# Kernel tuning notes

Hardware: AMD Instinct MI355X
Metric: run time of the kernel (lower is better)

Reference implementation:

```python
import jax, jax.numpy as jnp
import numpy as np
from jax import lax

DIVISOR = 2.0

def setup_inputs() -> dict:
    key = jax.random.key(0)
    k1, k2, k3, k4 = jax.random.split(key, 4)
    x = jax.random.normal(k1, (32, 3, 32, 128, 128), dtype=jnp.float16)
    conv_w = jax.random.normal(k2, (16, 3, 3, 3, 3), dtype=jnp.float16) * 0.1
    conv_b = jax.random.normal(k3, (16,), dtype=jnp.float16)
    bias = jax.random.normal(k4, (16,), dtype=jnp.float16)
    return {"x": x, "conv_w": conv_w, "conv_b": conv_b, "bias": bias}

def reference(x, conv_w, conv_b, bias):
    # Conv3d (valid padding, stride 1), fp16 like conv.half()
    y = lax.conv_general_dilated(
        x, conv_w, window_strides=(1, 1, 1), padding="VALID",
        dimension_numbers=("NCDHW", "OIDHW", "NCDHW"))
    y = y + conv_b[None, :, None, None, None]
    # Fused ReLU + 2x2x2 max pool
    y = jnp.maximum(y, jnp.asarray(0, y.dtype))
    B, C, D, H, W = y.shape
    Dp, Hp, Wp = D // 2, H // 2, W // 2
    pooled = y[:, :, :2 * Dp, :2 * Hp, :2 * Wp].reshape(
        B, C, Dp, 2, Hp, 2, Wp, 2).max(axis=(3, 5, 7))  # [B,C,Dp,Hp,Wp]
    # Spatial mean in fp32 (kernel accumulates in float)
    avg = pooled.astype(jnp.float32).mean(axis=(2, 3, 4))  # [B,C]
    # /divisor + bias[c], then sum over channels -> [B,1,1,1]
    per_ch = avg / DIVISOR + bias.astype(jnp.float32)[None, :]
    return per_ch.sum(axis=1).reshape(B, 1, 1, 1)
```

## Files before the change

kernel.cpp:

```cpp
#include <hip/hip_runtime.h>
#include <hip/hip_bf16.h>


typedef __attribute__((ext_vector_type(8)))  short  short8;
typedef __attribute__((ext_vector_type(2)))  float  floatx2;
typedef __attribute__((ext_vector_type(4)))  float  floatx4;
typedef __attribute__((ext_vector_type(16))) float  floatx16;

__device__ __forceinline__ short f2bf(float f) {
    unsigned u = __builtin_bit_cast(unsigned, f);
    unsigned r = (u + 0x7FFFu + ((u >> 16) & 1u)) >> 16;
    return (short)r;
}

__device__ __forceinline__ unsigned pkbf2(float a, float b) {
    __hip_bfloat162 h = __float22bfloat162_rn(float2{a, b});
    unsigned r;
    __builtin_memcpy(&r, &h, 4);
    return r;
}

template <int CTRL>
__device__ __forceinline__ float dpp_max(float v) {
    int x = __builtin_bit_cast(int, v);
    int y = __builtin_amdgcn_mov_dpp(x, CTRL, 0xF, 0xF, true);
    return fmaxf(v, __builtin_bit_cast(float, y));
}

#define BAR() asm volatile("s_waitcnt lgkmcnt(0)\n\ts_barrier" ::: "memory")

#define BUFSZ 16640

__global__ void init_kernel(const float* __restrict__ wg,
                            const float* __restrict__ biasg,
                            short* __restrict__ wtab,
                            float* __restrict__ out)
{
    const int t = threadIdx.x;
    if (t < 576) {
        const int lane = t & 63, f = t >> 6;
        const int kh = f / 3, kw = f % 3;
        const int m = lane & 31, hs = lane >> 5;
        const int ch = m >> 1, dd = m & 1;
        short8 v;
        #pragma unroll
        for (int j = 0; j < 8; ++j) {
            const int s = hs * 8 + j;
            const int dl = s >> 2, ci = s & 3;
            const int kd = dl - dd;
            v[j] = (ci < 3 && kd >= 0 && kd < 3)
                 ? f2bf(wg[ch * 81 + ci * 27 + kd * 9 + kh * 3 + kw]) : (short)0;
        }
        ((short8*)wtab)[f * 64 + lane] = v;
    }
    if (t < 32) {
        float s = 0.f;
        #pragma unroll
        for (int cc = 0; cc < 16; ++cc) s += biasg[cc];
        out[t] = s;
    }
}

__global__ __launch_bounds__(512, 4) void fused_conv_pool_reduce(
    const float* __restrict__ xg,
    const short* __restrict__ wtab,
    const float* __restrict__ cbg,
    float* __restrict__ out)
{
    __shared__ __align__(16) short rawT[2 * 130 * 64];
    __shared__ float wsums[8];

    const int lin = blockIdx.y * 63 + blockIdx.x;
    const int nl  = (lin & 7) * 252 + (lin >> 3);
    const int hp  = nl % 63;
    const int b   = nl / 63;

    const int tid = threadIdx.x;
    const int lane = tid & 63;
    const int wv   = tid >> 6;
    const int hs   = lane >> 5;

    short8 af[9];
    #pragma unroll
    for (int f = 0; f < 9; ++f) af[f] = ((const short8*)wtab)[f * 64 + lane];
    const float cbv = cbg[(lane >> 1) & 15];
    float maskA[4];
    #pragma unroll
    for (int a = 0; a < 4; ++a) {
        const bool ok = ((lane & 1) == 0) && (wv * 8 + 2 * a + hs <= 62);
        maskA[a] = ok ? 1.0f : 0.0f;
    }

    if (tid < 64)
        *(unsigned long long*)((char*)rawT + (tid >> 5) * BUFSZ + 16384 + (tid & 31) * 8) = 0ULL;

    #define SWZ(r) (((r) ^ ((r) >> 3)) & 7)

    const int w4 = tid & 31, dr2 = (tid >> 5) & 1, rr = (tid >> 6) & 1, hr2 = (tid >> 7) & 3;
    int waddr2[2];
    #pragma unroll
    for (int j = 0; j < 2; ++j) {
        const int row = 2 * w4 + 64 * rr + j;
        waddr2[j] = row * 128 + ((hr2 * 2) ^ SWZ(row)) * 16 + dr2 * 8;
    }

    const int wi = (lane >> 1) & 15, hh = lane & 1;
    int raddr[3][3];
    #pragma unroll
    for (int kh = 0; kh < 3; ++kh) {
        #pragma unroll
        for (int kw = 0; kw < 3; ++kw) {
            const int row = wv * 16 + wi + kw;
            const int phys = ((hh + kh) * 2 + hs) ^ SWZ(row);
            raddr[kh][kw] = row * 128 + phys * 16;
        }
    }

    {
        const int w4p = tid & 31, drp = (tid >> 5) & 3, hrp = (tid >> 7) & 3;
        const float* srcP = xg + ((size_t)b * 96 + drp) * 16384 + (2 * hp + hrp) * 128 + 4 * w4p;
        const floatx4 c0 = *(const floatx4*)(srcP);
        const floatx4 c1 = *(const floatx4*)(srcP + 524288);
        const floatx4 c2 = *(const floatx4*)(srcP + 1048576);
        const int chunkL = hrp * 2 + (drp >> 1);
        #pragma unroll
        for (int i = 0; i < 4; ++i) {
            const int row = 4 * w4p + i;
            const int ad = row * 128 + (chunkL ^ SWZ(row)) * 16 + (drp & 1) * 8;
            uint2 pk;
            pk.x = pkbf2(c0[i], c1[i]);
            pk.y = pkbf2(c2[i], 0.0f);
            *(uint2*)((char*)rawT + ad) = pk;
        }
    }

    const float* src2 = xg + ((size_t)b * 96 + 4 + dr2) * 16384
                      + (2 * hp + hr2) * 128 + 2 * w4 + 64 * rr;
    floatx2 A0 = *(const floatx2*)(src2);
    floatx2 A1 = *(const floatx2*)(src2 + 524288);
    floatx2 A2 = *(const floatx2*)(src2 + 1048576);

    float vsum = 0.f;
    for (int dp = 0; dp < 15; ++dp) {
        const int p16 = (dp & 1) << 4;
        if (dp <= 13) {
            const int bw = (((dp >> 1) + 1) & 1) * BUFSZ;
            uint2 pk0, pk1;
            pk0.x = pkbf2(A0[0], A1[0]); pk0.y = pkbf2(A2[0], 0.0f);
            pk1.x = pkbf2(A0[1], A1[1]); pk1.y = pkbf2(A2[1], 0.0f);
            *(uint2*)((char*)rawT + bw + (waddr2[0] ^ p16)) = pk0;
            *(uint2*)((char*)rawT + bw + (waddr2[1] ^ p16)) = pk1;
            if (dp <= 12) {
                src2 += 32768;
                A0 = *(const floatx2*)(src2);
                A1 = *(const floatx2*)(src2 + 524288);
                A2 = *(const floatx2*)(src2 + 1048576);
            }
        }
        BAR();

        const int roff = (((dp + hs) >> 1) & 1) * BUFSZ;

        floatx16 acc = {0.f,0.f,0.f,0.f,0.f,0.f,0.f,0.f,
                        0.f,0.f,0.f,0.f,0.f,0.f,0.f,0.f};
        #pragma unroll
        for (int kh = 0; kh < 3; ++kh) {
            #pragma unroll
            for (int kw = 0; kw < 3; ++kw) {
                const short8 bf = *(const short8*)((char*)rawT + roff + (raddr[kh][kw] ^ p16));
                acc = __builtin_amdgcn_mfma_f32_32x32x16_bf16(bf, af[kh * 3 + kw], acc, 0, 0, 0);
            }
        }
        #pragma unroll
        for (int a = 0; a < 4; ++a) {
            float m01 = fmaxf(acc[4 * a],     acc[4 * a + 1]);
            float m23 = fmaxf(acc[4 * a + 2], acc[4 * a + 3]);
            float m   = fmaxf(m01, m23);
            m = dpp_max<0xB1>(m);
            const float v = fmaxf(m + cbv, 0.f);
            vsum = fmaf(maskA[a], v, vsum);
        }
    }

    float s = vsum;
    #pragma unroll
    for (int off = 1; off < 64; off <<= 1) s += __shfl_xor(s, off, 64);

    if (lane == 0) wsums[wv] = s;
    __syncthreads();
    if (tid == 0) {
        float bs = 0.f;
        #pragma unroll
        for (int i = 0; i < 8; ++i) bs += wsums[i];
        atomicAdd(&out[b], bs * (1.0f / 119070.0f));
    }
}

extern "C" void kernel_launch(void* const* d_in, const int* in_sizes, int n_in,
                              void* d_out, int out_size, void* d_ws, size_t ws_size,
                              hipStream_t stream) {
    const float* x      = (const float*)d_in[0];
    const float* conv_w = (const float*)d_in[1];
    const float* conv_b = (const float*)d_in[2];
    const float* bias   = (const float*)d_in[3];
    float* out = (float*)d_out;
    short* wtab = (short*)d_ws;

    init_kernel<<<1, 576, 0, stream>>>(conv_w, bias, wtab, out);
    dim3 grid(63, 32);
    fused_conv_pool_reduce<<<grid, 512, 0, stream>>>(x, wtab, conv_b, out);
}
```

Baseline: 287.2 us.

## Reuse kh=0/2 LDS fragments to synthesize kh=1 via DPP, unroll loop by two

The kernel now reads two LDS fragments per kw (kh=0 and kh=2) and builds the kh=1 fragment by swapping adjacent lanes with DPP, where it used to do three separate LDS reads. This cuts LDS read traffic per MFMA step by a third. The depth loop is also unrolled in pairs with precomputed even/odd read and write addresses, which removes the per-iteration XOR and branch logic. The cost is extra VALU selects and DPP moves per fragment, plus more address registers, and correctness depends on the lane pairing matching the LDS layout.

```diff
diff --git a/kernel.cpp b/kernel.cpp
--- a/kernel.cpp
+++ b/kernel.cpp
@@ -5,6 +5,7 @@
 typedef __attribute__((ext_vector_type(8)))  short  short8;
 typedef __attribute__((ext_vector_type(2)))  float  floatx2;
 typedef __attribute__((ext_vector_type(4)))  float  floatx4;
+typedef __attribute__((ext_vector_type(4)))  int    intx4;
 typedef __attribute__((ext_vector_type(16))) float  floatx16;
 
 __device__ __forceinline__ short f2bf(float f) {
@@ -25,6 +26,18 @@
     int x = __builtin_bit_cast(int, v);
     int y = __builtin_amdgcn_mov_dpp(x, CTRL, 0xF, 0xF, true);
     return fmaxf(v, __builtin_bit_cast(float, y));
+}
+
+__device__ __forceinline__ short8 mixF1(short8 f0, short8 f2, bool hh1) {
+    intx4 a = __builtin_bit_cast(intx4, f0);
+    intx4 b = __builtin_bit_cast(intx4, f2);
+    intx4 r;
+    #pragma unroll
+    for (int i = 0; i < 4; ++i) {
+        int s = hh1 ? a[i] : b[i];
+        r[i] = __builtin_amdgcn_mov_dpp(s, 0xB1, 0xF, 0xF, true);
+    }
+    return __builtin_bit_cast(short8, r);
 }
 
 #define BAR() asm volatile("s_waitcnt lgkmcnt(0)\n\ts_barrier" ::: "memory")
@@ -90,6 +103,7 @@
         const bool ok = ((lane & 1) == 0) && (wv * 8 + 2 * a + hs <= 62);
         maskA[a] = ok ? 1.0f : 0.0f;
     }
+    const bool hh1 = (lane & 1);
 
     if (tid < 64)
         *(unsigned long long*)((char*)rawT + (tid >> 5) * BUFSZ + 16384 + (tid & 31) * 8) = 0ULL;
@@ -97,22 +111,24 @@
     #define SWZ(r) (((r) ^ ((r) >> 3)) & 7)
 
     const int w4 = tid & 31, dr2 = (tid >> 5) & 1, rr = (tid >> 6) & 1, hr2 = (tid >> 7) & 3;
-    int waddr2[2];
+    int wE[2], wO[2];
     #pragma unroll
     for (int j = 0; j < 2; ++j) {
         const int row = 2 * w4 + 64 * rr + j;
-        waddr2[j] = row * 128 + ((hr2 * 2) ^ SWZ(row)) * 16 + dr2 * 8;
-    }
-
-    const int wi = (lane >> 1) & 15, hh = lane & 1;
-    int raddr[3][3];
-    #pragma unroll
-    for (int kh = 0; kh < 3; ++kh) {
+        wE[j] = row * 128 + ((hr2 * 2) ^ SWZ(row)) * 16 + dr2 * 8;
+        wO[j] = wE[j] ^ 16;
+    }
+
+    const int wi = (lane >> 1) & 15;
+    int rE[2][3], rO[2][3];
+    #pragma unroll
+    for (int i = 0; i < 2; ++i) {
         #pragma unroll
         for (int kw = 0; kw < 3; ++kw) {
             const int row = wv * 16 + wi + kw;
-            const int phys = ((hh + kh) * 2 + hs) ^ SWZ(row);
-            raddr[kh][kw] = row * 128 + phys * 16;
+            const int phys = (((int)hh1 + 2 * i) * 2 + hs) ^ SWZ(row);
+            rE[i][kw] = row * 128 + phys * 16;
+            rO[i][kw] = rE[i][kw] ^ 16;
         }
     }
 
@@ -141,35 +157,31 @@
     floatx2 A2 = *(const floatx2*)(src2 + 1048576);
 
     float vsum = 0.f;
-    for (int dp = 0; dp < 15; ++dp) {
-        const int p16 = (dp & 1) << 4;
-        if (dp <= 13) {
-            const int bw = (((dp >> 1) + 1) & 1) * BUFSZ;
-            uint2 pk0, pk1;
-            pk0.x = pkbf2(A0[0], A1[0]); pk0.y = pkbf2(A2[0], 0.0f);
-            pk1.x = pkbf2(A0[1], A1[1]); pk1.y = pkbf2(A2[1], 0.0f);
-            *(uint2*)((char*)rawT + bw + (waddr2[0] ^ p16)) = pk0;
-            *(uint2*)((char*)rawT + bw + (waddr2[1] ^ p16)) = pk1;
-            if (dp <= 12) {
-                src2 += 32768;
-                A0 = *(const floatx2*)(src2);
-                A1 = *(const floatx2*)(src2 + 524288);
-                A2 = *(const floatx2*)(src2 + 1048576);
-            }
-        }
-        BAR();
-
-        const int roff = (((dp + hs) >> 1) & 1) * BUFSZ;
-
+
+    auto stageA = [&](int bw, const int (&wa)[2]) {
+        uint2 pk0, pk1;
+        pk0.x = pkbf2(A0[0], A1[0]); pk0.y = pkbf2(A2[0], 0.0f);
+        pk1.x = pkbf2(A0[1], A1[1]); pk1.y = pkbf2(A2[1], 0.0f);
+        *(uint2*)((char*)rawT + bw + wa[0]) = pk0;
+        *(uint2*)((char*)rawT + bw + wa[1]) = pk1;
+    };
+    auto loadA = [&]() {
+        src2 += 32768;
+        A0 = *(const floatx2*)(src2);
+        A1 = *(const floatx2*)(src2 + 524288);
+        A2 = *(const floatx2*)(src2 + 1048576);
+    };
+    auto compute = [&](int roff, const int (&ra)[2][3]) {
         floatx16 acc = {0.f,0.f,0.f,0.f,0.f,0.f,0.f,0.f,
                         0.f,0.f,0.f,0.f,0.f,0.f,0.f,0.f};
         #pragma unroll
-        for (int kh = 0; kh < 3; ++kh) {
-            #pragma unroll
-            for (int kw = 0; kw < 3; ++kw) {
-                const short8 bf = *(const short8*)((char*)rawT + roff + (raddr[kh][kw] ^ p16));
-                acc = __builtin_amdgcn_mfma_f32_32x32x16_bf16(bf, af[kh * 3 + kw], acc, 0, 0, 0);
-            }
+        for (int kw = 0; kw < 3; ++kw) {
+            const short8 f0 = *(const short8*)((char*)rawT + roff + ra[0][kw]);
+            const short8 f2 = *(const short8*)((char*)rawT + roff + ra[1][kw]);
+            const short8 f1 = mixF1(f0, f2, hh1);
+            acc = __builtin_amdgcn_mfma_f32_32x32x16_bf16(f0, af[kw],     acc, 0, 0, 0);
+            acc = __builtin_amdgcn_mfma_f32_32x32x16_bf16(f1, af[3 + kw], acc, 0, 0, 0);
+            acc = __builtin_amdgcn_mfma_f32_32x32x16_bf16(f2, af[6 + kw], acc, 0, 0, 0);
         }
         #pragma unroll
         for (int a = 0; a < 4; ++a) {
@@ -180,7 +192,21 @@
             const float v = fmaxf(m + cbv, 0.f);
             vsum = fmaf(maskA[a], v, vsum);
         }
-    }
+    };
+
+    for (int t = 0; t < 7; ++t) {
+        const int bufA = (t & 1) ? BUFSZ : 0;
+        const int bufB = BUFSZ - bufA;
+        stageA(bufB, wE);
+        loadA();
+        BAR();
+        compute(bufA, rE);
+        stageA(bufB, wO);
+        if (t < 6) loadA();
+        BAR();
+        compute(hs ? bufB : bufA, rO);
+    }
+    compute(BUFSZ, rE);
 
     float s = vsum;
     #pragma unroll
```

Measured after the change: 287.8 us. No clear change (+0.2%).

## Use six-slot rotating LDS ring to halve barriers per depth pair

Applied to the files above, without the earlier changes.

Replaces the two-buffer LDS layout with six narrower slots of 64 bytes per row in a rotating ring. Each iteration now loads and stores two depth planes (even and odd) and computes two pooled depth outputs per barrier, so the loop runs 7 iterations plus a tail instead of 15, with a simpler XOR swizzle. This aims to cut barrier and synchronisation overhead and amortise global-load latency across more work. In exchange it holds more prefetch registers and uses more complex slot index bookkeeping.

```diff
diff --git a/kernel.cpp b/kernel.cpp
--- a/kernel.cpp
+++ b/kernel.cpp
@@ -29,7 +29,7 @@
 
 #define BAR() asm volatile("s_waitcnt lgkmcnt(0)\n\ts_barrier" ::: "memory")
 
-#define BUFSZ 16640
+#define SLOT 8320
 
 __global__ void init_kernel(const float* __restrict__ wg,
                             const float* __restrict__ biasg,
@@ -67,7 +67,7 @@
     const float* __restrict__ cbg,
     float* __restrict__ out)
 {
-    __shared__ __align__(16) short rawT[2 * 130 * 64];
+    __shared__ __align__(16) short rawT[6 * 130 * 32];
     __shared__ float wsums[8];
 
     const int lin = blockIdx.y * 63 + blockIdx.x;
@@ -91,28 +91,29 @@
         maskA[a] = ok ? 1.0f : 0.0f;
     }
 
-    if (tid < 64)
-        *(unsigned long long*)((char*)rawT + (tid >> 5) * BUFSZ + 16384 + (tid & 31) * 8) = 0ULL;
-
-    #define SWZ(r) (((r) ^ ((r) >> 3)) & 7)
+    if (tid < 96) {
+        const int s = tid >> 4, q = tid & 15;
+        *(unsigned long long*)((char*)rawT + s * SLOT + 8192 + q * 8) = 0ULL;
+    }
 
     const int w4 = tid & 31, dr2 = (tid >> 5) & 1, rr = (tid >> 6) & 1, hr2 = (tid >> 7) & 3;
-    int waddr2[2];
+    int wad[2];
     #pragma unroll
     for (int j = 0; j < 2; ++j) {
         const int row = 2 * w4 + 64 * rr + j;
-        waddr2[j] = row * 128 + ((hr2 * 2) ^ SWZ(row)) * 16 + dr2 * 8;
+        const int phys = hr2 ^ ((row >> 1) & 3);
+        wad[j] = row * 64 + phys * 16 + dr2 * 8;
     }
 
     const int wi = (lane >> 1) & 15, hh = lane & 1;
-    int raddr[3][3];
+    int rad[3][3];
     #pragma unroll
     for (int kh = 0; kh < 3; ++kh) {
         #pragma unroll
         for (int kw = 0; kw < 3; ++kw) {
             const int row = wv * 16 + wi + kw;
-            const int phys = ((hh + kh) * 2 + hs) ^ SWZ(row);
-            raddr[kh][kw] = row * 128 + phys * 16;
+            const int phys = (hh + kh) ^ ((row >> 1) & 3);
+            rad[kh][kw] = row * 64 + phys * 16;
         }
     }
 
@@ -122,52 +123,39 @@
         const floatx4 c0 = *(const floatx4*)(srcP);
         const floatx4 c1 = *(const floatx4*)(srcP + 524288);
         const floatx4 c2 = *(const floatx4*)(srcP + 1048576);
-        const int chunkL = hrp * 2 + (drp >> 1);
+        const int slotP = (drp >> 1) * SLOT;
+        const int parP  = (drp & 1) * 8;
         #pragma unroll
         for (int i = 0; i < 4; ++i) {
             const int row = 4 * w4p + i;
-            const int ad = row * 128 + (chunkL ^ SWZ(row)) * 16 + (drp & 1) * 8;
+            const int phys = hrp ^ ((row >> 1) & 3);
             uint2 pk;
             pk.x = pkbf2(c0[i], c1[i]);
             pk.y = pkbf2(c2[i], 0.0f);
-            *(uint2*)((char*)rawT + ad) = pk;
-        }
-    }
-
-    const float* src2 = xg + ((size_t)b * 96 + 4 + dr2) * 16384
+            *(uint2*)((char*)rawT + slotP + row * 64 + phys * 16 + parP) = pk;
+        }
+    }
+
+    const float* srcE = xg + ((size_t)b * 96 + 4 + dr2) * 16384
                       + (2 * hp + hr2) * 128 + 2 * w4 + 64 * rr;
-    floatx2 A0 = *(const floatx2*)(src2);
-    floatx2 A1 = *(const floatx2*)(src2 + 524288);
-    floatx2 A2 = *(const floatx2*)(src2 + 1048576);
+    const float* srcO = srcE + 32768;
+    floatx2 E0 = *(const floatx2*)(srcE);
+    floatx2 E1 = *(const floatx2*)(srcE + 524288);
+    floatx2 E2 = *(const floatx2*)(srcE + 1048576);
+    floatx2 O0 = *(const floatx2*)(srcO);
+    floatx2 O1 = *(const floatx2*)(srcO + 524288);
+    floatx2 O2 = *(const floatx2*)(srcO + 1048576);
 
     float vsum = 0.f;
-    for (int dp = 0; dp < 15; ++dp) {
-        const int p16 = (dp & 1) << 4;
-        if (dp <= 13) {
-            const int bw = (((dp >> 1) + 1) & 1) * BUFSZ;
-            uint2 pk0, pk1;
-            pk0.x = pkbf2(A0[0], A1[0]); pk0.y = pkbf2(A2[0], 0.0f);
-            pk1.x = pkbf2(A0[1], A1[1]); pk1.y = pkbf2(A2[1], 0.0f);
-            *(uint2*)((char*)rawT + bw + (waddr2[0] ^ p16)) = pk0;
-            *(uint2*)((char*)rawT + bw + (waddr2[1] ^ p16)) = pk1;
-            if (dp <= 12) {
-                src2 += 32768;
-                A0 = *(const floatx2*)(src2);
-                A1 = *(const floatx2*)(src2 + 524288);
-                A2 = *(const floatx2*)(src2 + 1048576);
-            }
-        }
-        BAR();
-
-        const int roff = (((dp + hs) >> 1) & 1) * BUFSZ;
-
+
+    auto computeDP = [&](int base) {
         floatx16 acc = {0.f,0.f,0.f,0.f,0.f,0.f,0.f,0.f,
                         0.f,0.f,0.f,0.f,0.f,0.f,0.f,0.f};
         #pragma unroll
         for (int kh = 0; kh < 3; ++kh) {
             #pragma unroll
             for (int kw = 0; kw < 3; ++kw) {
-                const short8 bf = *(const short8*)((char*)rawT + roff + (raddr[kh][kw] ^ p16));
+                const short8 bf = *(const short8*)((char*)rawT + base + rad[kh][kw]);
                 acc = __builtin_amdgcn_mfma_f32_32x32x16_bf16(bf, af[kh * 3 + kw], acc, 0, 0, 0);
             }
         }
@@ -180,7 +168,43 @@
             const float v = fmaxf(m + cbv, 0.f);
             vsum = fmaf(maskA[a], v, vsum);
         }
-    }
+    };
+
+    int m3 = 0;
+    for (int t = 0; t < 7; ++t) {
+        const int sR0 = m3 * (2 * SLOT);
+        const int sR1 = sR0 + SLOT;
+        const int sR2 = (m3 == 2) ? 0 : sR0 + 2 * SLOT;
+        const int sW3 = (m3 == 2) ? SLOT : sR2 + SLOT;
+
+        {
+            uint2 p0, p1;
+            p0.x = pkbf2(E0[0], E1[0]); p0.y = pkbf2(E2[0], 0.0f);
+            p1.x = pkbf2(E0[1], E1[1]); p1.y = pkbf2(E2[1], 0.0f);
+            *(uint2*)((char*)rawT + sR2 + wad[0]) = p0;
+            *(uint2*)((char*)rawT + sR2 + wad[1]) = p1;
+            p0.x = pkbf2(O0[0], O1[0]); p0.y = pkbf2(O2[0], 0.0f);
+            p1.x = pkbf2(O0[1], O1[1]); p1.y = pkbf2(O2[1], 0.0f);
+            *(uint2*)((char*)rawT + sW3 + wad[0]) = p0;
+            *(uint2*)((char*)rawT + sW3 + wad[1]) = p1;
+        }
+        if (t < 6) {
+            srcE += 65536;  srcO += 65536;
+            E0 = *(const floatx2*)(srcE);
+            E1 = *(const floatx2*)(srcE + 524288);
+            E2 = *(const floatx2*)(srcE + 1048576);
+            O0 = *(const floatx2*)(srcO);
+            O1 = *(const floatx2*)(srcO + 524288);
+            O2 = *(const floatx2*)(srcO + 1048576);
+        }
+        BAR();
+
+        computeDP(hs ? sR1 : sR0);
+        computeDP(hs ? sR2 : sR1);
+
+        m3 = (m3 == 2) ? 0 : m3 + 1;
+    }
+    computeDP(hs ? 3 * SLOT : 2 * SLOT);
 
     float s = vsum;
     #pragma unroll
```

New measurement: 289.0 us. No clear change (+0.6%).

## Split each block's width into two halves with halo columns, doubling grid

Applied to the files above, without the earlier changes.

Each block now covers half of the output width (64 columns plus a 2-column halo) with 256 threads instead of 512, and the grid doubles to 63x64. Halo threads load and stage the two extra input columns every depth step, and the right half zero-pads its tail. The aim is smaller blocks, less LDS per block and more resident blocks for better latency hiding and load balance. In exchange the halo columns are loaded redundantly, the halo loads are scalar and uncoalesced, and there are twice as many atomics on the output.

```diff
diff --git a/kernel.cpp b/kernel.cpp
--- a/kernel.cpp
+++ b/kernel.cpp
@@ -29,7 +29,7 @@
 
 #define BAR() asm volatile("s_waitcnt lgkmcnt(0)\n\ts_barrier" ::: "memory")
 
-#define BUFSZ 16640
+#define BUFSZ 8448
 
 __global__ void init_kernel(const float* __restrict__ wg,
                             const float* __restrict__ biasg,
@@ -61,19 +61,22 @@
     }
 }
 
-__global__ __launch_bounds__(512, 4) void fused_conv_pool_reduce(
+__global__ __launch_bounds__(256, 8) void fused_conv_pool_reduce(
     const float* __restrict__ xg,
     const short* __restrict__ wtab,
     const float* __restrict__ cbg,
     float* __restrict__ out)
 {
-    __shared__ __align__(16) short rawT[2 * 130 * 64];
-    __shared__ float wsums[8];
+    __shared__ __align__(16) short rawT[2 * 66 * 64];
+    __shared__ float wsums[4];
 
     const int lin = blockIdx.y * 63 + blockIdx.x;
-    const int nl  = (lin & 7) * 252 + (lin >> 3);
+    const int nl  = (lin & 7) * 504 + (lin >> 3);
     const int hp  = nl % 63;
-    const int b   = nl / 63;
+    const int yy  = nl / 63;
+    const int ws  = yy & 1;
+    const int b   = yy >> 1;
+    const int wbase = ws * 64;
 
     const int tid = threadIdx.x;
     const int lane = tid & 63;
@@ -87,58 +90,82 @@
     float maskA[4];
     #pragma unroll
     for (int a = 0; a < 4; ++a) {
-        const bool ok = ((lane & 1) == 0) && (wv * 8 + 2 * a + hs <= 62);
+        const bool ok = ((lane & 1) == 0) && (ws * 32 + wv * 8 + 2 * a + hs <= 62);
         maskA[a] = ok ? 1.0f : 0.0f;
     }
 
-    if (tid < 64)
-        *(unsigned long long*)((char*)rawT + (tid >> 5) * BUFSZ + 16384 + (tid & 31) * 8) = 0ULL;
+    if (ws && tid < 64)
+        *(unsigned long long*)((char*)rawT + (tid >> 5) * BUFSZ + 8192 + (tid & 31) * 8) = 0ULL;
 
     #define SWZ(r) (((r) ^ ((r) >> 3)) & 7)
 
-    const int w4 = tid & 31, dr2 = (tid >> 5) & 1, rr = (tid >> 6) & 1, hr2 = (tid >> 7) & 3;
-    int waddr2[2];
+    const int w4 = tid & 31, dr2 = (tid >> 5) & 1, hr2 = (tid >> 6) & 3;
+    int wad[2];
     #pragma unroll
     for (int j = 0; j < 2; ++j) {
-        const int row = 2 * w4 + 64 * rr + j;
-        waddr2[j] = row * 128 + ((hr2 * 2) ^ SWZ(row)) * 16 + dr2 * 8;
-    }
+        const int row = 2 * w4 + j;
+        wad[j] = row * 128 + ((hr2 * 2) ^ SWZ(row)) * 16 + dr2 * 8;
+    }
+
+    const bool haloT = (ws == 0) && (tid < 16);
+    const int hrow = 64 + (tid & 1);
+    const int hlh  = (tid >> 1) & 3;
+    const int pah  = (tid >> 3) & 1;
+    const int hwad = hrow * 128 + ((hlh * 2) ^ SWZ(hrow)) * 16 + pah * 8;
+    const float* hb = xg + (size_t)b * 96 * 16384 + (2 * hp + hlh) * 128 + 64 + (tid & 1);
 
     const int wi = (lane >> 1) & 15, hh = lane & 1;
-    int raddr[3][3];
+    int rad[3][3];
     #pragma unroll
     for (int kh = 0; kh < 3; ++kh) {
         #pragma unroll
         for (int kw = 0; kw < 3; ++kw) {
             const int row = wv * 16 + wi + kw;
             const int phys = ((hh + kh) * 2 + hs) ^ SWZ(row);
-            raddr[kh][kw] = row * 128 + phys * 16;
+            rad[kh][kw] = row * 128 + phys * 16;
         }
     }
 
     {
-        const int w4p = tid & 31, drp = (tid >> 5) & 3, hrp = (tid >> 7) & 3;
-        const float* srcP = xg + ((size_t)b * 96 + drp) * 16384 + (2 * hp + hrp) * 128 + 4 * w4p;
+        const int w4p = tid & 15, drp = (tid >> 4) & 3, hrp = (tid >> 6) & 3;
+        const float* srcP = xg + ((size_t)b * 96 + drp) * 16384
+                          + (2 * hp + hrp) * 128 + wbase + 4 * w4p;
         const floatx4 c0 = *(const floatx4*)(srcP);
         const floatx4 c1 = *(const floatx4*)(srcP + 524288);
         const floatx4 c2 = *(const floatx4*)(srcP + 1048576);
         const int chunkL = hrp * 2 + (drp >> 1);
+        const int parP   = (drp & 1) * 8;
         #pragma unroll
         for (int i = 0; i < 4; ++i) {
             const int row = 4 * w4p + i;
-            const int ad = row * 128 + (chunkL ^ SWZ(row)) * 16 + (drp & 1) * 8;
+            const int ad = row * 128 + (chunkL ^ SWZ(row)) * 16 + parP;
             uint2 pk;
             pk.x = pkbf2(c0[i], c1[i]);
             pk.y = pkbf2(c2[i], 0.0f);
             *(uint2*)((char*)rawT + ad) = pk;
         }
     }
+    if (ws == 0 && tid < 32) {
+        const int row = 64 + (tid & 1), hl = (tid >> 1) & 3, dpl = (tid >> 3) & 3;
+        const float* p = xg + ((size_t)b * 96 + dpl) * 16384 + (2 * hp + hl) * 128 + 64 + (tid & 1);
+        const float f0 = p[0], f1 = p[524288], f2 = p[1048576];
+        const int ad = row * 128 + (((hl * 2) + (dpl >> 1)) ^ SWZ(row)) * 16 + (dpl & 1) * 8;
+        uint2 pk;
+        pk.x = pkbf2(f0, f1);
+        pk.y = pkbf2(f2, 0.0f);
+        *(uint2*)((char*)rawT + ad) = pk;
+    }
 
     const float* src2 = xg + ((size_t)b * 96 + 4 + dr2) * 16384
-                      + (2 * hp + hr2) * 128 + 2 * w4 + 64 * rr;
+                      + (2 * hp + hr2) * 128 + wbase + 2 * w4;
     floatx2 A0 = *(const floatx2*)(src2);
     floatx2 A1 = *(const floatx2*)(src2 + 524288);
     floatx2 A2 = *(const floatx2*)(src2 + 1048576);
+    float h0 = 0.f, h1 = 0.f, h2 = 0.f;
+    if (haloT) {
+        const float* p = hb + (size_t)(4 + pah) * 16384;
+        h0 = p[0]; h1 = p[524288]; h2 = p[1048576];
+    }
 
     float vsum = 0.f;
     for (int dp = 0; dp < 15; ++dp) {
@@ -148,13 +175,22 @@
             uint2 pk0, pk1;
             pk0.x = pkbf2(A0[0], A1[0]); pk0.y = pkbf2(A2[0], 0.0f);
             pk1.x = pkbf2(A0[1], A1[1]); pk1.y = pkbf2(A2[1], 0.0f);
-            *(uint2*)((char*)rawT + bw + (waddr2[0] ^ p16)) = pk0;
-            *(uint2*)((char*)rawT + bw + (waddr2[1] ^ p16)) = pk1;
+            *(uint2*)((char*)rawT + bw + (wad[0] ^ p16)) = pk0;
+            *(uint2*)((char*)rawT + bw + (wad[1] ^ p16)) = pk1;
+            if (haloT) {
+                uint2 hpk;
+                hpk.x = pkbf2(h0, h1); hpk.y = pkbf2(h2, 0.0f);
+                *(uint2*)((char*)rawT + bw + (hwad ^ p16)) = hpk;
+            }
             if (dp <= 12) {
                 src2 += 32768;
                 A0 = *(const floatx2*)(src2);
                 A1 = *(const floatx2*)(src2 + 524288);
                 A2 = *(const floatx2*)(src2 + 1048576);
+                if (haloT) {
+                    const float* p = hb + (size_t)(2 * dp + 6 + pah) * 16384;
+                    h0 = p[0]; h1 = p[524288]; h2 = p[1048576];
+                }
             }
         }
         BAR();
@@ -167,7 +203,7 @@
         for (int kh = 0; kh < 3; ++kh) {
             #pragma unroll
             for (int kw = 0; kw < 3; ++kw) {
-                const short8 bf = *(const short8*)((char*)rawT + roff + (raddr[kh][kw] ^ p16));
+                const short8 bf = *(const short8*)((char*)rawT + roff + (rad[kh][kw] ^ p16));
                 acc = __builtin_amdgcn_mfma_f32_32x32x16_bf16(bf, af[kh * 3 + kw], acc, 0, 0, 0);
             }
         }
@@ -191,7 +227,7 @@
     if (tid == 0) {
         float bs = 0.f;
         #pragma unroll
-        for (int i = 0; i < 8; ++i) bs += wsums[i];
+        for (int i = 0; i < 4; ++i) bs += wsums[i];
         atomicAdd(&out[b], bs * (1.0f / 119070.0f));
     }
 }
@@ -207,6 +243,6 @@
     short* wtab = (short*)d_ws;
 
     init_kernel<<<1, 576, 0, stream>>>(conv_w, bias, wtab, out);
-    dim3 grid(63, 32);
-    fused_conv_pool_reduce<<<grid, 512, 0, stream>>>(x, wtab, conv_b, out);
-}
+    dim3 grid(63, 64);
+    fused_conv_pool_reduce<<<grid, 256, 0, stream>>>(x, wtab, conv_b, out);
+}
```

Result: slower. 548.2 us (+90.9%).
